# Kernel optimization log

Measured on AMD Instinct MI355X. Metric: run time of the kernel, lower is better.

Reference implementation:

```python
import jax, jax.numpy as jnp
import numpy as np

N_QUBITS = 12
N_LAYERS = 4


def rot_mat(phi, theta, omega):
    # PennyLane Rot(phi,theta,omega) = RZ(omega) @ RY(theta) @ RZ(phi)
    c = jnp.cos(theta / 2).astype(jnp.complex64)
    s = jnp.sin(theta / 2).astype(jnp.complex64)
    ep = jnp.exp(-1j * (phi + omega) / 2).astype(jnp.complex64)
    em = jnp.exp(1j * (phi - omega) / 2).astype(jnp.complex64)
    return jnp.stack([
        jnp.stack([ep * c, -em * s]),
        jnp.stack([jnp.conj(em) * s, jnp.conj(ep) * c]),
    ])  # (2,2) complex64


def apply_1q(state, U, w):
    # state: (batch, 2, 2, ..., 2) with N_QUBITS qubit axes
    s = jnp.moveaxis(state, w + 1, 1)
    s = jnp.einsum('ij,bj...->bi...', U, s)
    return jnp.moveaxis(s, 1, w + 1)


def apply_cnot(state, c, t):
    s = jnp.moveaxis(state, (c + 1, t + 1), (1, 2))
    s = jnp.concatenate([s[:, :1], s[:, 1:, ::-1]], axis=1)  # flip target where control=1
    return jnp.moveaxis(s, (1, 2), (c + 1, t + 1))


def setup_inputs() -> dict:
    key = jax.random.key(0)
    ks = jax.random.split(key, 6)
    L, F, n = 128, 96, N_QUBITS
    x = jax.random.normal(ks[0], (64, L, 32), dtype=jnp.float32)
    W_in = jax.random.normal(ks[1], (2 ** n, L), dtype=jnp.float32) * 0.05
    b_in = jax.random.normal(ks[2], (2 ** n,), dtype=jnp.float32) * 0.05
    q_weights = jax.random.uniform(ks[3], (N_LAYERS, n, 3), dtype=jnp.float32,
                                   minval=0.0, maxval=2.0 * np.pi)
    W_out = jax.random.normal(ks[4], (F, n), dtype=jnp.float32) * 0.1
    b_out = jax.random.normal(ks[5], (F,), dtype=jnp.float32) * 0.1
    return {"x": x, "W_in": W_in, "b_in": b_in, "q_weights": q_weights,
            "W_out": W_out, "b_out": b_out}


def reference(x, W_in, b_in, q_weights, W_out, b_out):
    n = N_QUBITS
    B, L, M = x.shape
    h = x.transpose(0, 2, 1).reshape(B * M, L)
    h = h @ W_in.T + b_in + 1e-6
    # AmplitudeEmbedding with normalize=True
    h = h / jnp.linalg.norm(h, axis=1, keepdims=True)
    state = h.astype(jnp.complex64).reshape((B * M,) + (2,) * n)
    # StronglyEntanglingLayers: per layer Rot on every wire, then CNOT ring with range r
    for l in range(N_LAYERS):
        for w in range(n):
            U = rot_mat(q_weights[l, w, 0], q_weights[l, w, 1], q_weights[l, w, 2])
            state = apply_1q(state, U, w)
        r = l % (n - 1) + 1
        for w in range(n):
            state = apply_cnot(state, w, (w + r) % n)
    probs = state.real ** 2 + state.imag ** 2  # (BM, 2,...,2)
    zs = []
    for i in range(n):
        axes = tuple(a for a in range(1, n + 1) if a != i + 1)
        p = probs.sum(axis=axes)  # (BM, 2)
        zs.append(p[:, 0] - p[:, 1])
    z = jnp.stack(zs, axis=1)  # (BM, n) expvals of PauliZ
    out = z @ W_out.T + b_out  # (BM, F)
    return out.reshape(B, M, -1).transpose(0, 2, 1)  # (B, F, M)
```

## Files before the change

kernel.cpp:

```cpp
#include <hip/hip_runtime.h>
#include <math.h>

#define NQ 12
#define DIM 4096
#define NSAMP 2048
#define NLAYERS 4

typedef _Float16 h8v __attribute__((ext_vector_type(8)));
typedef short s8v __attribute__((ext_vector_type(8)));
typedef float f4v __attribute__((ext_vector_type(4)));

struct QMasks { unsigned short mv[NLAYERS][12]; };

static void cnot_masks(int l, unsigned* m) {
    int r = l % (NQ - 1) + 1;
    for (int j = 0; j < NQ; ++j) {
        unsigned v = 1u << j;
        for (int k = NQ - 1; k >= 0; --k) {
            int c = k, t = (k + r) % NQ;
            int pc = NQ - 1 - c, pt = NQ - 1 - t;
            if ((v >> pc) & 1u) v ^= (1u << pt);
        }
        m[j] = v;
    }
}

static QMasks host_masks() {
    QMasks Q{};
    for (int l = 0; l < NLAYERS; ++l) {
        unsigned m[12];
        cnot_masks(l, m);
        unsigned A[12], I[12];
        for (int k = 0; k < 12; ++k) {
            unsigned row = 0;
            for (int j = 0; j < 12; ++j) row |= ((m[j] >> k) & 1u) << j;
            A[k] = row; I[k] = 1u << k;
        }
        for (int c = 0; c < 12; ++c) {
            int p = c; while (!((A[p] >> c) & 1u)) ++p;
            unsigned ta = A[p], ti = I[p]; A[p] = A[c]; I[p] = I[c]; A[c] = ta; I[c] = ti;
            for (int r2 = 0; r2 < 12; ++r2)
                if (r2 != c && ((A[r2] >> c) & 1u)) { A[r2] ^= A[c]; I[r2] ^= I[c]; }
        }
        for (int j = 0; j < 12; ++j) {
            unsigned colv = 0;
            for (int k = 0; k < 12; ++k) colv |= ((I[k] >> j) & 1u) << k;
            Q.mv[l][j] = (unsigned short)colv;
        }
    }
    return Q;
}

__device__ __forceinline__ unsigned short f2bf(float f) {
    unsigned u = __builtin_bit_cast(unsigned, f);
    return (unsigned short)((u + 0x7FFFu + ((u >> 16) & 1u)) >> 16);
}
__device__ __forceinline__ float bf2f(unsigned short b) {
    unsigned u = ((unsigned)b) << 16;
    return __builtin_bit_cast(float, u);
}
__device__ __forceinline__ unsigned packh(float re, float im) {
    unsigned short rb = __builtin_bit_cast(unsigned short, (_Float16)re);
    unsigned short ib = __builtin_bit_cast(unsigned short, (_Float16)im);
    return (unsigned)rb | ((unsigned)ib << 16);
}
__device__ __forceinline__ float h2f(unsigned short h) {
    return (float)__builtin_bit_cast(_Float16, h);
}

#define LDA 72
__global__ __launch_bounds__(256) void gemm_in_mfma(
        const float* __restrict__ x, const float* __restrict__ Win,
        const float* __restrict__ bin, const float* __restrict__ qw,
        unsigned short* __restrict__ h16, h8v* __restrict__ gates) {
    __shared__ unsigned short Ah[64 * LDA], Al[64 * LDA];
    __shared__ unsigned short Bh[64 * LDA], Bl[64 * LDA];
    const int tid = threadIdx.x;

    if (blockIdx.y == 32) {
        const int s = blockIdx.x;
        if (s >= 12 || tid >= 64) return;
        const int layer = s / 3, sg = s % 3;
        const int row = tid & 15, hi = tid >> 4;
        float ur[4][2][2], ui[4][2][2];
        for (int t = 0; t < 4; ++t) {
            const float* q = qw + (layer * NQ + sg * 4 + t) * 3;
            float sn, cs, sa, ca, sb, cb;
            sincosf(0.5f * q[1], &sn, &cs);
            sincosf(0.5f * (q[0] + q[2]), &sa, &ca);
            sincosf(0.5f * (q[0] - q[2]), &sb, &cb);
            ur[t][0][0] =  cs * ca; ui[t][0][0] = -cs * sa;
            ur[t][0][1] = -sn * cb; ui[t][0][1] = -sn * sb;
            ur[t][1][0] =  sn * cb; ui[t][1][0] = -sn * sb;
            ur[t][1][1] =  cs * ca; ui[t][1][1] =  cs * sa;
        }
        h8v arh, arl, aih, ail;
        for (int mm = 0; mm < 4; ++mm) {
            int m = hi * 4 + mm;
            float gr = 1.f, gi = 0.f;
            for (int t = 0; t < 4; ++t) {
                int rb = (row >> (3 - t)) & 1, cb2 = (m >> (3 - t)) & 1;
                float ar = ur[t][rb][cb2], ai = ui[t][rb][cb2];
                float nr = gr * ar - gi * ai, ni = gr * ai + gi * ar;
                gr = nr; gi = ni;
            }
            float vv[4] = {gr, -gi, gi, gr};
            _Float16 hh;
            hh = (_Float16)vv[0]; arh[2*mm]   = hh; arl[2*mm]   = (_Float16)(vv[0] - (float)hh);
            hh = (_Float16)vv[1]; arh[2*mm+1] = hh; arl[2*mm+1] = (_Float16)(vv[1] - (float)hh);
            hh = (_Float16)vv[2]; aih[2*mm]   = hh; ail[2*mm]   = (_Float16)(vv[2] - (float)hh);
            hh = (_Float16)vv[3]; aih[2*mm+1] = hh; ail[2*mm+1] = (_Float16)(vv[3] - (float)hh);
        }
        gates[(s * 4 + 0) * 64 + tid] = arh;
        gates[(s * 4 + 1) * 64 + tid] = arl;
        gates[(s * 4 + 2) * 64 + tid] = aih;
        gates[(s * 4 + 3) * 64 + tid] = ail;
        return;
    }

    const int kBase = blockIdx.x * 64;
    const int sBase = blockIdx.y * 64;
    const int lane = tid & 63, wid = tid >> 6;
    const int wr = wid >> 1, wc = wid & 1;
    const int l16 = lane & 15, lg = lane >> 4;
    const int xbase = (sBase >> 5) * 4096;
    f4v acc[2][2] = {};

#pragma unroll 1
    for (int ch = 0; ch < 2; ++ch) {
        __syncthreads();
#pragma unroll
        for (int it = 0; it < 4; ++it) {
            int idx = it * 256 + tid;
            int row = idx >> 4, c4 = (idx & 15) * 4;
            const float4 w = *(const float4*)&Win[(kBase + row) * 128 + ch * 64 + c4];
            ushort4 hi4, lo4;
            hi4.x = f2bf(w.x); lo4.x = f2bf(w.x - bf2f(hi4.x));
            hi4.y = f2bf(w.y); lo4.y = f2bf(w.y - bf2f(hi4.y));
            hi4.z = f2bf(w.z); lo4.z = f2bf(w.z - bf2f(hi4.z));
            hi4.w = f2bf(w.w); lo4.w = f2bf(w.w - bf2f(hi4.w));
            *(ushort4*)&Ah[row * LDA + c4] = hi4;
            *(ushort4*)&Al[row * LDA + c4] = lo4;
        }
#pragma unroll
        for (int it = 0; it < 16; ++it) {
            int idx = it * 256 + tid;
            int srow = idx & 63, l = idx >> 6;
            float val = x[xbase + (srow >> 5) * 4096 + (ch * 64 + l) * 32 + (srow & 31)];
            unsigned short hv = f2bf(val);
            Bh[srow * LDA + l] = hv;
            Bl[srow * LDA + l] = f2bf(val - bf2f(hv));
        }
        __syncthreads();
#pragma unroll
        for (int kk = 0; kk < 2; ++kk) {
            s8v ah[2], al2[2], bh[2], bl[2];
#pragma unroll
            for (int r = 0; r < 2; ++r) {
                int row = wr * 32 + r * 16 + l16;
                ah[r]  = *(s8v*)&Ah[row * LDA + kk * 32 + lg * 8];
                al2[r] = *(s8v*)&Al[row * LDA + kk * 32 + lg * 8];
            }
#pragma unroll
            for (int c = 0; c < 2; ++c) {
                int col = wc * 32 + c * 16 + l16;
                bh[c] = *(s8v*)&Bh[col * LDA + kk * 32 + lg * 8];
                bl[c] = *(s8v*)&Bl[col * LDA + kk * 32 + lg * 8];
            }
#pragma unroll
            for (int r = 0; r < 2; ++r)
#pragma unroll
                for (int c = 0; c < 2; ++c) {
                    acc[r][c] = __builtin_amdgcn_mfma_f32_16x16x32_bf16(ah[r],  bh[c], acc[r][c], 0, 0, 0);
                    acc[r][c] = __builtin_amdgcn_mfma_f32_16x16x32_bf16(ah[r],  bl[c], acc[r][c], 0, 0, 0);
                    acc[r][c] = __builtin_amdgcn_mfma_f32_16x16x32_bf16(al2[r], bh[c], acc[r][c], 0, 0, 0);
                }
        }
    }
#pragma unroll
    for (int r = 0; r < 2; ++r) {
        const int kg = kBase + wr * 32 + r * 16 + lg * 4;
        const float4 b4 = *(const float4*)&bin[kg];
#pragma unroll
        for (int c = 0; c < 2; ++c) {
            const int sg2 = sBase + wc * 32 + c * 16 + l16;
            ushort4 o;
            o.x = __builtin_bit_cast(unsigned short, (_Float16)(acc[r][c][0] + b4.x + 1e-6f));
            o.y = __builtin_bit_cast(unsigned short, (_Float16)(acc[r][c][1] + b4.y + 1e-6f));
            o.z = __builtin_bit_cast(unsigned short, (_Float16)(acc[r][c][2] + b4.z + 1e-6f));
            o.w = __builtin_bit_cast(unsigned short, (_Float16)(acc[r][c][3] + b4.w + 1e-6f));
            *(ushort4*)&h16[(size_t)sg2 * 4096 + kg] = o;
        }
    }
}

#define ST 20u

__global__ __launch_bounds__(256, 4) void qsim_mfma(
        const unsigned short* __restrict__ h16, const h8v* __restrict__ gates,
        const float* __restrict__ Wout, const float* __restrict__ bout,
        float* __restrict__ out, QMasks Q) {
    __shared__ __align__(16) unsigned lds[256 * 20];
    __shared__ float red[4];
    __shared__ float wred[4][13];
    __shared__ float zsh[13];

    const int tid = threadIdx.x;
    const int samp = blockIdx.x;
    const int lane = tid & 63;
    const int wv = tid >> 6;
    const int l16 = tid & 15;
    const int hi = (tid >> 4) & 3;
    const f4v fz = {0.f, 0.f, 0.f, 0.f};

    float vr[16]; float ss = 0.f;
#pragma unroll
    for (int j = 0; j < 16; ++j) {
        float f = h2f(h16[samp * DIM + j * 256 + tid]);
        vr[j] = f; ss += f * f;
    }
#pragma unroll
    for (int o = 32; o > 0; o >>= 1) ss += __shfl_xor(ss, o);
    if (lane == 0) red[wv] = ss;
    __syncthreads();
    const float inv = 1.0f / sqrtf(red[0] + red[1] + red[2] + red[3]);
#pragma unroll
    for (int q = 0; q < 4; ++q) {
        uint4 w;
        w.x = packh(vr[4 * q + 0] * inv, 0.f);
        w.y = packh(vr[4 * q + 1] * inv, 0.f);
        w.z = packh(vr[4 * q + 2] * inv, 0.f);
        w.w = packh(vr[4 * q + 3] * inv, 0.f);
        *(uint4*)&lds[tid * ST + 4 * q] = w;
    }
    __syncthreads();

    h8v ArH, ArL, AiH, AiL;
    f4v dre0, dre1, dre2, dre3, dim0, dim1, dim2, dim3;

#define LOAD_FRAGS(S) { const h8v* gp = gates + (S) * 256 + lane;             \
    ArH = gp[0]; ArL = gp[64]; AiH = gp[128]; AiL = gp[192]; }

#define TC(T, DRE, DIM) {                                                     \
    unsigned ra = ((unsigned)(((4 * wv + (T)) << 4) | l16)) * ST + (unsigned)(hi << 2); \
    h8v bf = __builtin_bit_cast(h8v, *(const uint4*)&lds[ra]);                \
    DRE = __builtin_amdgcn_mfma_f32_16x16x32_f16(ArH, bf, fz, 0, 0, 0);       \
    DRE = __builtin_amdgcn_mfma_f32_16x16x32_f16(ArL, bf, DRE, 0, 0, 0);      \
    DIM = __builtin_amdgcn_mfma_f32_16x16x32_f16(AiH, bf, fz, 0, 0, 0);       \
    DIM = __builtin_amdgcn_mfma_f32_16x16x32_f16(AiL, bf, DIM, 0, 0, 0); }

#define COMPUTE4                                                              \
    TC(0, dre0, dim0) TC(1, dre1, dim1) TC(2, dre2, dim2) TC(3, dre3, dim3)   \
    __syncthreads();

#define WS0REG(R, OFF) {                                                      \
    uint4 w;                                                                  \
    w.x = packh(dre0[R], dim0[R]); w.y = packh(dre1[R], dim1[R]);             \
    w.z = packh(dre2[R], dim2[R]); w.w = packh(dre3[R], dim3[R]);             \
    *(uint4*)&lds[wb0 + (OFF)] = w; }
#define WS0 {                                                                 \
    unsigned wb0 = 1280u * hi + ST * (unsigned)l16 + 4u * wv;                 \
    WS0REG(0, 0) WS0REG(1, 320) WS0REG(2, 640) WS0REG(3, 960) }               \
    __syncthreads();

#define WS1T(T, DRE, DIM) {                                                   \
    unsigned wa = 320u * (unsigned)(4 * wv + (T)) + 80u * hi + (unsigned)l16; \
    lds[wa]      = packh(DRE[0], DIM[0]);                                     \
    lds[wa + 20] = packh(DRE[1], DIM[1]);                                     \
    lds[wa + 40] = packh(DRE[2], DIM[2]);                                     \
    lds[wa + 60] = packh(DRE[3], DIM[3]); }
#define WS1 { WS1T(0, dre0, dim0) WS1T(1, dre1, dim1)                         \
              WS1T(2, dre2, dim2) WS1T(3, dre3, dim3) }                       \
    __syncthreads();

#define X3T(L, T, DRE, DIM) {                                                 \
    unsigned bb = bb0;                                                        \
    if ((T) & 1) bb ^= Q.mv[L][8];                                            \
    if ((T) & 2) bb ^= Q.mv[L][9];                                            \
    unsigned b0 = bb, b1 = bb ^ Q.mv[L][0];                                   \
    unsigned b2 = bb ^ Q.mv[L][1], b3 = b1 ^ Q.mv[L][1];                      \
    lds[(b0 & 255u) * ST + (b0 >> 8)] = packh(DRE[0], DIM[0]);                \
    lds[(b1 & 255u) * ST + (b1 >> 8)] = packh(DRE[1], DIM[1]);                \
    lds[(b2 & 255u) * ST + (b2 >> 8)] = packh(DRE[2], DIM[2]);                \
    lds[(b3 & 255u) * ST + (b3 >> 8)] = packh(DRE[3], DIM[3]); }
#define WX3(L) {                                                              \
    unsigned bb0 = 0;                                                         \
    if (hi & 1)  bb0 ^= Q.mv[L][2];  if (hi & 2)  bb0 ^= Q.mv[L][3];          \
    if (l16 & 1) bb0 ^= Q.mv[L][4];  if (l16 & 2) bb0 ^= Q.mv[L][5];          \
    if (l16 & 4) bb0 ^= Q.mv[L][6];  if (l16 & 8) bb0 ^= Q.mv[L][7];          \
    if (wv & 1)  bb0 ^= Q.mv[L][10]; if (wv & 2)  bb0 ^= Q.mv[L][11];         \
    X3T(L, 0, dre0, dim0) X3T(L, 1, dre1, dim1)                               \
    X3T(L, 2, dre2, dim2) X3T(L, 3, dre3, dim3) }                             \
    __syncthreads();

#define RUN_LAYER(L)                                                          \
    LOAD_FRAGS(3 * (L) + 0) COMPUTE4 WS0                                      \
    LOAD_FRAGS(3 * (L) + 1) COMPUTE4 WS1                                      \
    LOAD_FRAGS(3 * (L) + 2) COMPUTE4 WX3(L)

    RUN_LAYER(0)
    RUN_LAYER(1)
    RUN_LAYER(2)
    RUN_LAYER(3)

    float P = 0.f;
    float z03[4] = {0.f, 0.f, 0.f, 0.f};
#pragma unroll
    for (int j = 0; j < 16; ++j) {
        unsigned w = lds[tid * ST + j];
        float re = h2f((unsigned short)(w & 0xFFFFu));
        float im = h2f((unsigned short)(w >> 16));
        float pr = re * re + im * im;
        P += pr;
#pragma unroll
        for (int i = 0; i < 4; ++i)
            z03[i] += ((j >> (3 - i)) & 1) ? -pr : pr;
    }
    float zv[12];
#pragma unroll
    for (int i = 0; i < 4; ++i) zv[i] = z03[i];
#pragma unroll
    for (int i = 4; i < 12; ++i)
        zv[i] = ((tid >> (11 - i)) & 1) ? -P : P;
#pragma unroll
    for (int i = 0; i < 12; ++i) {
        float z = zv[i];
#pragma unroll
        for (int o = 32; o > 0; o >>= 1) z += __shfl_xor(z, o);
        if (lane == 0) wred[wv][i] = z;
    }
    {
        float v = P;
#pragma unroll
        for (int o = 32; o > 0; o >>= 1) v += __shfl_xor(v, o);
        if (lane == 0) wred[wv][12] = v;
    }
    __syncthreads();
    if (tid < 13)
        zsh[tid] = wred[0][tid] + wred[1][tid] + wred[2][tid] + wred[3][tid];
    __syncthreads();

    if (tid < 96) {
        const float invP = 1.0f / zsh[12];
        float acc = bout[tid];
#pragma unroll
        for (int i = 0; i < 12; ++i) acc += zsh[i] * invP * Wout[tid * 12 + i];
        int b = samp >> 5, m = samp & 31;
        out[b * (96 * 32) + tid * 32 + m] = acc;
    }
}

extern "C" void kernel_launch(void* const* d_in, const int* in_sizes, int n_in,
                              void* d_out, int out_size, void* d_ws, size_t ws_size,
                              hipStream_t stream) {
    const float* x    = (const float*)d_in[0];
    const float* Win  = (const float*)d_in[1];
    const float* bin  = (const float*)d_in[2];
    const float* qw   = (const float*)d_in[3];
    const float* Wout = (const float*)d_in[4];
    const float* bout = (const float*)d_in[5];
    unsigned short* h16 = (unsigned short*)d_ws;
    h8v* gates = (h8v*)((char*)d_ws + (size_t)NSAMP * DIM * 2);

    QMasks Q = host_masks();

    gemm_in_mfma<<<dim3(64, 33), 256, 0, stream>>>(x, Win, bin, qw, h16, gates);
    qsim_mfma<<<dim3(NSAMP), 256, 0, stream>>>(h16, gates, Wout, bout,
                                               (float*)d_out, Q);
}
```

Baseline: 77.04 us.

## Double-buffer LDS state to halve barriers per gate stage

The state vector in LDS is now ping-ponged between two buffers, so each compute stage reads one buffer and writes the other. That removes the barrier between the MFMA reads and the scatter writes, leaving one __syncthreads per stage instead of two. The final probability readout also switches from scalar to 128-bit LDS loads, and the reduction scratch is aliased into the second buffer, which needs an extra barrier. LDS use doubles and launch bounds drop from 4 to 2 blocks per SM, which may lower occupancy.

```diff
diff --git a/kernel.cpp b/kernel.cpp
--- a/kernel.cpp
+++ b/kernel.cpp
@@ -195,15 +195,16 @@
 }
 
 #define ST 20u
-
-__global__ __launch_bounds__(256, 4) void qsim_mfma(
+#define BUFW 5120
+
+__global__ __launch_bounds__(256, 2) void qsim_mfma(
         const unsigned short* __restrict__ h16, const h8v* __restrict__ gates,
         const float* __restrict__ Wout, const float* __restrict__ bout,
         float* __restrict__ out, QMasks Q) {
-    __shared__ __align__(16) unsigned lds[256 * 20];
-    __shared__ float red[4];
-    __shared__ float wred[4][13];
-    __shared__ float zsh[13];
+    __shared__ __align__(16) unsigned lds[2 * BUFW];
+    float* red        = (float*)&lds[BUFW];
+    float (*wred)[13] = (float(*)[13])&lds[BUFW + 8];
+    float* zsh        = (float*)&lds[BUFW + 80];
 
     const int tid = threadIdx.x;
     const int samp = blockIdx.x;
@@ -216,7 +217,7 @@
     float vr[16]; float ss = 0.f;
 #pragma unroll
     for (int j = 0; j < 16; ++j) {
-        float f = h2f(h16[samp * DIM + j * 256 + tid]);
+        float f = h2f(h16[(size_t)samp * DIM + j * 256 + tid]);
         vr[j] = f; ss += f * f;
     }
 #pragma unroll
@@ -241,80 +242,84 @@
 #define LOAD_FRAGS(S) { const h8v* gp = gates + (S) * 256 + lane;             \
     ArH = gp[0]; ArL = gp[64]; AiH = gp[128]; AiL = gp[192]; }
 
-#define TC(T, DRE, DIM) {                                                     \
-    unsigned ra = ((unsigned)(((4 * wv + (T)) << 4) | l16)) * ST + (unsigned)(hi << 2); \
+#define TC(RB, T, DRE, DIM) {                                                 \
+    unsigned ra = (RB) + ((unsigned)(((4 * wv + (T)) << 4) | l16)) * ST       \
+                + (unsigned)(hi << 2);                                        \
     h8v bf = __builtin_bit_cast(h8v, *(const uint4*)&lds[ra]);                \
     DRE = __builtin_amdgcn_mfma_f32_16x16x32_f16(ArH, bf, fz, 0, 0, 0);       \
     DRE = __builtin_amdgcn_mfma_f32_16x16x32_f16(ArL, bf, DRE, 0, 0, 0);      \
     DIM = __builtin_amdgcn_mfma_f32_16x16x32_f16(AiH, bf, fz, 0, 0, 0);       \
     DIM = __builtin_amdgcn_mfma_f32_16x16x32_f16(AiL, bf, DIM, 0, 0, 0); }
 
-#define COMPUTE4                                                              \
-    TC(0, dre0, dim0) TC(1, dre1, dim1) TC(2, dre2, dim2) TC(3, dre3, dim3)   \
-    __syncthreads();
-
-#define WS0REG(R, OFF) {                                                      \
-    uint4 w;                                                                  \
-    w.x = packh(dre0[R], dim0[R]); w.y = packh(dre1[R], dim1[R]);             \
-    w.z = packh(dre2[R], dim2[R]); w.w = packh(dre3[R], dim3[R]);             \
-    *(uint4*)&lds[wb0 + (OFF)] = w; }
-#define WS0 {                                                                 \
-    unsigned wb0 = 1280u * hi + ST * (unsigned)l16 + 4u * wv;                 \
-    WS0REG(0, 0) WS0REG(1, 320) WS0REG(2, 640) WS0REG(3, 960) }               \
-    __syncthreads();
-
-#define WS1T(T, DRE, DIM) {                                                   \
-    unsigned wa = 320u * (unsigned)(4 * wv + (T)) + 80u * hi + (unsigned)l16; \
+#define COMPUTE4(RB)                                                          \
+    TC(RB, 0, dre0, dim0) TC(RB, 1, dre1, dim1)                               \
+    TC(RB, 2, dre2, dim2) TC(RB, 3, dre3, dim3)
+
+#define WS0(WB) {                                                             \
+    unsigned wb0 = (WB) + 1280u * hi + ST * (unsigned)l16 + 4u * wv;          \
+    _Pragma("unroll")                                                         \
+    for (int r = 0; r < 4; ++r) {                                             \
+        uint4 v;                                                              \
+        v.x = packh(dre0[r], dim0[r]); v.y = packh(dre1[r], dim1[r]);         \
+        v.z = packh(dre2[r], dim2[r]); v.w = packh(dre3[r], dim3[r]);         \
+        *(uint4*)&lds[wb0 + 320u * r] = v; } }
+
+#define WS1T(WB, T, DRE, DIM) {                                               \
+    unsigned wa = (WB) + 320u * (unsigned)(4 * wv + (T)) + 80u * hi           \
+                + (unsigned)l16;                                              \
     lds[wa]      = packh(DRE[0], DIM[0]);                                     \
     lds[wa + 20] = packh(DRE[1], DIM[1]);                                     \
     lds[wa + 40] = packh(DRE[2], DIM[2]);                                     \
     lds[wa + 60] = packh(DRE[3], DIM[3]); }
-#define WS1 { WS1T(0, dre0, dim0) WS1T(1, dre1, dim1)                         \
-              WS1T(2, dre2, dim2) WS1T(3, dre3, dim3) }                       \
-    __syncthreads();
-
-#define X3T(L, T, DRE, DIM) {                                                 \
+#define WS1(WB) { WS1T(WB, 0, dre0, dim0) WS1T(WB, 1, dre1, dim1)             \
+                  WS1T(WB, 2, dre2, dim2) WS1T(WB, 3, dre3, dim3) }
+
+#define X3T(WB, L, T, DRE, DIM) {                                             \
     unsigned bb = bb0;                                                        \
     if ((T) & 1) bb ^= Q.mv[L][8];                                            \
     if ((T) & 2) bb ^= Q.mv[L][9];                                            \
     unsigned b0 = bb, b1 = bb ^ Q.mv[L][0];                                   \
     unsigned b2 = bb ^ Q.mv[L][1], b3 = b1 ^ Q.mv[L][1];                      \
-    lds[(b0 & 255u) * ST + (b0 >> 8)] = packh(DRE[0], DIM[0]);                \
-    lds[(b1 & 255u) * ST + (b1 >> 8)] = packh(DRE[1], DIM[1]);                \
-    lds[(b2 & 255u) * ST + (b2 >> 8)] = packh(DRE[2], DIM[2]);                \
-    lds[(b3 & 255u) * ST + (b3 >> 8)] = packh(DRE[3], DIM[3]); }
-#define WX3(L) {                                                              \
+    lds[(WB) + (b0 & 255u) * ST + (b0 >> 8)] = packh(DRE[0], DIM[0]);         \
+    lds[(WB) + (b1 & 255u) * ST + (b1 >> 8)] = packh(DRE[1], DIM[1]);         \
+    lds[(WB) + (b2 & 255u) * ST + (b2 >> 8)] = packh(DRE[2], DIM[2]);         \
+    lds[(WB) + (b3 & 255u) * ST + (b3 >> 8)] = packh(DRE[3], DIM[3]); }
+#define WX3(WB, L) {                                                          \
     unsigned bb0 = 0;                                                         \
     if (hi & 1)  bb0 ^= Q.mv[L][2];  if (hi & 2)  bb0 ^= Q.mv[L][3];          \
     if (l16 & 1) bb0 ^= Q.mv[L][4];  if (l16 & 2) bb0 ^= Q.mv[L][5];          \
     if (l16 & 4) bb0 ^= Q.mv[L][6];  if (l16 & 8) bb0 ^= Q.mv[L][7];          \
     if (wv & 1)  bb0 ^= Q.mv[L][10]; if (wv & 2)  bb0 ^= Q.mv[L][11];         \
-    X3T(L, 0, dre0, dim0) X3T(L, 1, dre1, dim1)                               \
-    X3T(L, 2, dre2, dim2) X3T(L, 3, dre3, dim3) }                             \
-    __syncthreads();
-
-#define RUN_LAYER(L)                                                          \
-    LOAD_FRAGS(3 * (L) + 0) COMPUTE4 WS0                                      \
-    LOAD_FRAGS(3 * (L) + 1) COMPUTE4 WS1                                      \
-    LOAD_FRAGS(3 * (L) + 2) COMPUTE4 WX3(L)
-
-    RUN_LAYER(0)
-    RUN_LAYER(1)
-    RUN_LAYER(2)
-    RUN_LAYER(3)
+    X3T(WB, L, 0, dre0, dim0) X3T(WB, L, 1, dre1, dim1)                       \
+    X3T(WB, L, 2, dre2, dim2) X3T(WB, L, 3, dre3, dim3) }
+
+#define RUN_LAYER(L, A, B)                                                    \
+    LOAD_FRAGS(3 * (L) + 0) COMPUTE4(A) WS0(B)    __syncthreads();            \
+    LOAD_FRAGS(3 * (L) + 1) COMPUTE4(B) WS1(A)    __syncthreads();            \
+    LOAD_FRAGS(3 * (L) + 2) COMPUTE4(A) WX3(B, L) __syncthreads();
+
+    RUN_LAYER(0, 0, BUFW)
+    RUN_LAYER(1, BUFW, 0)
+    RUN_LAYER(2, 0, BUFW)
+    RUN_LAYER(3, BUFW, 0)
 
     float P = 0.f;
     float z03[4] = {0.f, 0.f, 0.f, 0.f};
 #pragma unroll
-    for (int j = 0; j < 16; ++j) {
-        unsigned w = lds[tid * ST + j];
-        float re = h2f((unsigned short)(w & 0xFFFFu));
-        float im = h2f((unsigned short)(w >> 16));
-        float pr = re * re + im * im;
-        P += pr;
-#pragma unroll
-        for (int i = 0; i < 4; ++i)
-            z03[i] += ((j >> (3 - i)) & 1) ? -pr : pr;
+    for (int g = 0; g < 4; ++g) {
+        uint4 u4 = *(const uint4*)&lds[tid * ST + 4 * g];
+        unsigned uu[4] = {u4.x, u4.y, u4.z, u4.w};
+#pragma unroll
+        for (int e = 0; e < 4; ++e) {
+            const int j = 4 * g + e;
+            float re = h2f((unsigned short)(uu[e] & 0xFFFFu));
+            float im = h2f((unsigned short)(uu[e] >> 16));
+            float pr = re * re + im * im;
+            P += pr;
+#pragma unroll
+            for (int i = 0; i < 4; ++i)
+                z03[i] += ((j >> (3 - i)) & 1) ? -pr : pr;
+        }
     }
     float zv[12];
 #pragma unroll
@@ -322,6 +327,7 @@
 #pragma unroll
     for (int i = 4; i < 12; ++i)
         zv[i] = ((tid >> (11 - i)) & 1) ? -P : P;
+    __syncthreads();
 #pragma unroll
     for (int i = 0; i < 12; ++i) {
         float z = zv[i];
```

New measurement: 75.59 us. Within noise of the previous version (-1.9%).
